# Performance work log

Hardware: AMD Instinct MI355X
Metric: run time of the kernel (lower is better)

## Reference

```python
import jax, jax.numpy as jnp
import numpy as np

N_NODES = 50000
N_EDGES = 800000
FEAT = 128
HID = 128
NUM_GRAPHS = 64
ODE_STEPS = 8   # fixed-step RK4 stand-in for adaptive odeint over CFG.ode_time_points
DEPTH = 1.0
EPS = 1e-5


def layer_norm(x, g, b):
    m = jnp.mean(x, axis=-1, keepdims=True)
    v = jnp.var(x, axis=-1, keepdims=True)
    return (x - m) * jax.lax.rsqrt(v + EPS) * g + b


def setup_inputs() -> dict:
    key = jax.random.key(0)
    ks = jax.random.split(key, 16)
    s = 1.0 / np.sqrt(FEAT)
    sh = 1.0 / np.sqrt(HID)
    inp = {
        "x": jax.random.normal(ks[0], (N_NODES, FEAT), jnp.float32),
        "edge_index": jax.random.randint(ks[1], (2, N_EDGES), 0, N_NODES, jnp.int64),
        "batch": jnp.sort(jax.random.randint(ks[2], (N_NODES,), 0, NUM_GRAPHS, jnp.int64)),
        "alpha": jnp.float32(0.8),
        "beta": jnp.float32(0.6),
        "phase": jnp.float32(0.7),
        "W_in": jax.random.normal(ks[3], (FEAT, HID), jnp.float32) * s,
        "b_in": jnp.zeros((HID,), jnp.float32),
        "g_in": jnp.ones((HID,), jnp.float32),
        "be_in": jnp.zeros((HID,), jnp.float32),
        "W_alt": jax.random.normal(ks[4], (FEAT, HID), jnp.float32) * s,
        "b_alt": jnp.zeros((HID,), jnp.float32),
        "g_alt": jnp.ones((HID,), jnp.float32),
        "be_alt": jnp.zeros((HID,), jnp.float32),
        "W_self": jax.random.normal(ks[5], (HID, HID), jnp.float32) * sh,
        "W_msg": jax.random.normal(ks[6], (HID, HID), jnp.float32) * sh,
        "b_ode": jnp.zeros((HID,), jnp.float32),
        "W_int": jax.random.normal(ks[7], (2 * HID, HID), jnp.float32) * sh / np.sqrt(2.0),
        "b_int": jnp.zeros((HID,), jnp.float32),
        "g_int": jnp.ones((HID,), jnp.float32),
        "be_int": jnp.zeros((HID,), jnp.float32),
        "W_out": jax.random.normal(ks[8], (HID, HID), jnp.float32) * sh,
        "b_out": jnp.zeros((HID,), jnp.float32),
    }
    return inp


def _forward(x, alpha, beta, phase,
             W_in, b_in, g_in, be_in,
             W_alt, b_alt, g_alt, be_alt,
             W_self, W_msg, b_ode,
             W_int, b_int, g_int, be_int,
             W_out, b_out,
             edge_index, batch):
    src, dst = edge_index[0], edge_index[1]
    # in-degree for mean aggregation (clamped to 1)
    deg = jax.ops.segment_sum(jnp.ones((src.shape[0],), jnp.float32), dst,
                              num_segments=N_NODES)
    deg = jnp.maximum(deg, 1.0)[:, None]

    # quantum amplitudes -> measurement probabilities (normalized)
    norm = jnp.sqrt(alpha ** 2 + beta ** 2)
    a, b = alpha / norm, beta / norm
    p0, p1 = a ** 2, b ** 2

    # two projection pathways in superposition
    h0 = jax.nn.gelu(layer_norm(x @ W_in + b_in, g_in, be_in))
    h1 = jax.nn.gelu(layer_norm(x @ W_alt + b_alt, g_alt, be_alt))
    h = jnp.sqrt(p0) * h0 + jnp.sqrt(p1) * h1  # [N, H]

    # Neural ODE: dh/dt = tanh(h W_self + mean_{j->i}(h_j W_msg) + b)
    def ode_f(h):
        msg = h[src] @ W_msg                       # [E, H] gather + GEMM
        agg = jax.ops.segment_sum(msg, dst, num_segments=N_NODES) / deg
        return jnp.tanh(h @ W_self + agg + b_ode)

    dt = jnp.float32(DEPTH / ODE_STEPS)

    def rk4_step(h, _):
        k1 = ode_f(h)
        k2 = ode_f(h + 0.5 * dt * k1)
        k3 = ode_f(h + 0.5 * dt * k2)
        k4 = ode_f(h + dt * k3)
        return h + (dt / 6.0) * (k1 + 2.0 * k2 + 2.0 * k3 + k4), None

    h, _ = jax.lax.scan(rk4_step, h, None, length=ODE_STEPS)

    # quantum interference mixing (conditional branch -> masked add)
    interf = 2.0 * jnp.sqrt(p0 * p1) * jnp.cos(phase)
    h_int = jnp.tanh(layer_norm(jnp.concatenate([h, h], axis=-1) @ W_int + b_int,
                                g_int, be_int))
    gate = jnp.where(jnp.abs(interf) > 0.01, interf, 0.0)
    h = h + gate * h_int

    # eval-mode collapse: if p1 >= p0, scale by Re(e^{i*phase}) = cos(phase)
    h = jnp.where(p0 > p1, h, h * jnp.cos(phase))

    h_out = h @ W_out + b_out

    # global mean pool over graphs
    cnt = jax.ops.segment_sum(jnp.ones((N_NODES,), jnp.float32), batch,
                              num_segments=NUM_GRAPHS)
    pooled = jax.ops.segment_sum(h_out, batch, num_segments=NUM_GRAPHS)
    return pooled / jnp.maximum(cnt, 1.0)[:, None]  # [NUM_GRAPHS, H]


def reference(x, edge_index, batch, alpha, beta, phase,
              W_in, b_in, g_in, be_in,
              W_alt, b_alt, g_alt, be_alt,
              W_self, W_msg, b_ode,
              W_int, b_int, g_int, be_int,
              W_out, b_out):
    return _forward(x, alpha, beta, phase,
                    W_in, b_in, g_in, be_in,
                    W_alt, b_alt, g_alt, be_alt,
                    W_self, W_msg, b_ode,
                    W_int, b_int, g_int, be_int,
                    W_out, b_out, edge_index, batch)
```

## Files before the change

kernel.cpp:

```cpp
#include <hip/hip_runtime.h>
#include <math.h>

#define NND 50000
#define NED 800000
#define HD  128
#define NG  64
#define MT  32

typedef __attribute__((ext_vector_type(8))) short short8v;
typedef __attribute__((ext_vector_type(4))) float float4v;
typedef __attribute__((ext_vector_type(2))) float float2v;

__device__ __forceinline__ float gelu_t(float x) {
  const float c = 0.7978845608028654f;
  float t = tanhf(c * (x + 0.044715f * x * x * x));
  return 0.5f * x * (1.0f + t);
}

__device__ __forceinline__ unsigned short f2bf(float f) {
  unsigned int u = __float_as_uint(f);
  u += 0x7FFFu + ((u >> 16) & 1u);
  return (unsigned short)(u >> 16);
}
__device__ __forceinline__ float bf2f(unsigned short s) {
  return __uint_as_float(((unsigned int)s) << 16);
}
__device__ __forceinline__ float bflo(unsigned int u) { return __uint_as_float(u << 16); }
__device__ __forceinline__ float bfhi(unsigned int u) { return __uint_as_float(u & 0xFFFF0000u); }
__device__ __forceinline__ unsigned char f2fp8(float f) {
  return (unsigned char)(__builtin_amdgcn_cvt_pk_fp8_f32(f, f, 0, false) & 0xFF);
}

__global__ void k_hist(const int* __restrict__ dst, int* __restrict__ degi) {
  int e = blockIdx.x * 256 + threadIdx.x;
  if (e < NED) atomicAdd(&degi[dst[e]], 1);
}

__global__ __launch_bounds__(1024) void k_scan(
    const int* __restrict__ degi, int* __restrict__ rowptr,
    int* __restrict__ cursor, float* __restrict__ deginv) {
  __shared__ int wsum[16];
  int tid = threadIdx.x;
  int lane = tid & 63;
  int wid = tid >> 6;
  int running = 0;
  for (int base = 0; base < NND; base += 1024) {
    int idx = base + tid;
    int v = (idx < NND) ? degi[idx] : 0;
    int s = v;
#pragma unroll
    for (int o = 1; o < 64; o <<= 1) {
      int t = __shfl_up(s, o, 64);
      if (lane >= o) s += t;
    }
    if (lane == 63) wsum[wid] = s;
    __syncthreads();
    if (wid == 0) {
      int ws = (lane < 16) ? wsum[lane] : 0;
#pragma unroll
      for (int o = 1; o < 16; o <<= 1) {
        int t = __shfl_up(ws, o, 64);
        if (lane >= o) ws += t;
      }
      if (lane < 16) wsum[lane] = ws;
    }
    __syncthreads();
    int woff = wid ? wsum[wid - 1] : 0;
    int excl = running + woff + s - v;
    if (idx < NND) {
      rowptr[idx] = excl;
      cursor[idx] = excl;
      deginv[idx] = 1.0f / (float)max(v, 1);
    }
    int tot = wsum[15];
    __syncthreads();
    running += tot;
  }
  if (tid == 0) rowptr[NND] = running;
}

__global__ void k_scatter(const int* __restrict__ src, const int* __restrict__ dst,
                          int* __restrict__ cursor, unsigned short* __restrict__ cs16) {
  int e = blockIdx.x * 256 + threadIdx.x;
  if (e < NED) {
    int d = dst[e];
    int pos = atomicAdd(&cursor[d], 1);
    cs16[pos] = (unsigned short)src[e];
  }
}

__global__ void k_cnt(const int* __restrict__ batch, float* __restrict__ cnt) {
  int g = threadIdx.x;
  if (g >= NG) return;
  int lo, hi, ub_g, ub_gm1;
  lo = 0; hi = NND;
  while (lo < hi) { int mid = (lo + hi) >> 1; if (batch[mid] <= g) lo = mid + 1; else hi = mid; }
  ub_g = lo;
  if (g == 0) ub_gm1 = 0;
  else {
    lo = 0; hi = NND;
    int v = g - 1;
    while (lo < hi) { int mid = (lo + hi) >> 1; if (batch[mid] <= v) lo = mid + 1; else hi = mid; }
    ub_gm1 = lo;
  }
  cnt[g] = (float)(ub_g - ub_gm1);
}

__global__ void k_weff(const float* __restrict__ Wint, float* __restrict__ weff) {
  int i = blockIdx.x * 256 + threadIdx.x;
  if (i < HD * HD) weff[i] = Wint[i] + Wint[i + HD * HD];
}

__global__ void k_prepB(const float* __restrict__ Wself, const float* __restrict__ Wmsg,
                        unsigned short* __restrict__ Bt) {
  int i = blockIdx.x * 256 + threadIdx.x;
  if (i < 128 * 256) {
    int n = i >> 8, k = i & 255;
    float w = (k < HD) ? Wself[k * HD + n] : Wmsg[(k - HD) * HD + n];
    Bt[i] = f2bf(w);
  }
}

__global__ void k_prepIn(const float* __restrict__ Win, const float* __restrict__ Walt,
                         unsigned short* __restrict__ BtIn) {
  int i = blockIdx.x * 256 + threadIdx.x;
  if (i < 2 * 128 * 128) {
    int p = i >> 14; int rem = i & 16383; int n = rem >> 7; int k = rem & 127;
    const float* W = p ? Walt : Win;
    BtIn[i] = f2bf(W[k * 128 + n]);
  }
}

__global__ __launch_bounds__(256) void k_init2(
    const float* __restrict__ x, const unsigned short* __restrict__ BtIn,
    const float* __restrict__ bin, const float* __restrict__ gin, const float* __restrict__ bein,
    const float* __restrict__ balt, const float* __restrict__ galt, const float* __restrict__ bealt,
    const float* __restrict__ alphap, const float* __restrict__ betap,
    unsigned short* __restrict__ hbf)
{
  __shared__ float red[4][16][2];
  __shared__ unsigned short gtile[2][16][64];
  int tid = threadIdx.x;
  int wave = tid >> 6;
  int lane = tid & 63;
  int l15 = lane & 15;
  int lhi = lane >> 4;
  int path = wave >> 1;
  int colBase = (wave & 1) * 64;
  int rowBase = blockIdx.x * 64;

  const unsigned short* Bp = BtIn + path * 128 * 128;
  short8v bfr[4][4];
#pragma unroll
  for (int t = 0; t < 4; ++t) {
    int n = colBase + t * 16 + l15;
#pragma unroll
    for (int s = 0; s < 4; ++s)
      bfr[t][s] = *(const short8v*)&Bp[n * 128 + s * 32 + lhi * 8];
  }

  const float* bvp = path ? balt : bin;
  const float* gp  = path ? galt : gin;
  const float* bep = path ? bealt : bein;
  float bv[4], gw[4], bew[4];
#pragma unroll
  for (int t = 0; t < 4; ++t) {
    int col = colBase + t * 16 + l15;
    bv[t] = bvp[col]; gw[t] = gp[col]; bew[t] = bep[col];
  }

  float al = alphap[0], btv = betap[0];
  float nrm = sqrtf(al * al + btv * btv);
  float w0 = fabsf(al) / nrm, w1 = fabsf(btv) / nrm;

  for (int rt = 0; rt < 4; ++rt) {
    int arow = rowBase + rt * 16 + l15; if (arow >= NND) arow = NND - 1;
    short8v afr[4];
#pragma unroll
    for (int s = 0; s < 4; ++s) {
      float4 xa = *(const float4*)&x[(size_t)arow * HD + s * 32 + lhi * 8];
      float4 xb = *(const float4*)&x[(size_t)arow * HD + s * 32 + lhi * 8 + 4];
      short8v f;
      f[0] = (short)f2bf(xa.x); f[1] = (short)f2bf(xa.y);
      f[2] = (short)f2bf(xa.z); f[3] = (short)f2bf(xa.w);
      f[4] = (short)f2bf(xb.x); f[5] = (short)f2bf(xb.y);
      f[6] = (short)f2bf(xb.z); f[7] = (short)f2bf(xb.w);
      afr[s] = f;
    }

    float4v acc[4];
#pragma unroll
    for (int t = 0; t < 4; ++t) acc[t] = (float4v){0.f, 0.f, 0.f, 0.f};
#pragma unroll
    for (int s = 0; s < 4; ++s) {
#pragma unroll
      for (int t = 0; t < 4; ++t)
        acc[t] = __builtin_amdgcn_mfma_f32_16x16x32_bf16(afr[s], bfr[t][s], acc[t], 0, 0, 0);
    }

    float z[4][4];
    float psum[4], psq[4];
#pragma unroll
    for (int r = 0; r < 4; ++r) {
      float s1 = 0.f, s2 = 0.f;
#pragma unroll
      for (int t = 0; t < 4; ++t) {
        float zz = acc[t][r] + bv[t];
        z[r][t] = zz;
        s1 += zz; s2 += zz * zz;
      }
#pragma unroll
      for (int m = 1; m < 16; m <<= 1) {
        s1 += __shfl_xor(s1, m, 16);
        s2 += __shfl_xor(s2, m, 16);
      }
      psum[r] = s1; psq[r] = s2;
    }
    if (l15 == 0) {
#pragma unroll
      for (int r = 0; r < 4; ++r) {
        red[wave][lhi * 4 + r][0] = psum[r];
        red[wave][lhi * 4 + r][1] = psq[r];
      }
    }
    __syncthreads();

    int pw = wave ^ 1;
    float gval[4][4];
#pragma unroll
    for (int r = 0; r < 4; ++r) {
      int rowl = lhi * 4 + r;
      float S = psum[r] + red[pw][rowl][0];
      float Q = psq[r]  + red[pw][rowl][1];
      float mean = S * (1.0f / 128.0f);
      float var  = Q * (1.0f / 128.0f) - mean * mean;
      float rs = rsqrtf(var + 1e-5f);
#pragma unroll
      for (int t = 0; t < 4; ++t)
        gval[r][t] = gelu_t((z[r][t] - mean) * rs * gw[t] + bew[t]);
    }

    if (path == 1) {
#pragma unroll
      for (int r = 0; r < 4; ++r)
#pragma unroll
        for (int t = 0; t < 4; ++t)
          gtile[wave & 1][lhi * 4 + r][t * 16 + l15] = f2bf(gval[r][t]);
    }
    __syncthreads();

    if (path == 0) {
#pragma unroll
      for (int r = 0; r < 4; ++r) {
        int m = rowBase + rt * 16 + lhi * 4 + r;
        if (m < NND) {
#pragma unroll
          for (int t = 0; t < 4; ++t) {
            float g1 = bf2f(gtile[wave & 1][lhi * 4 + r][t * 16 + l15]);
            float hv = w0 * gval[r][t] + w1 * g1;
            hbf[(size_t)m * HD + colBase + t * 16 + l15] = f2bf(hv);
          }
        }
      }
    }
    __syncthreads();
  }
}

__global__ __launch_bounds__(256) void k_gath2(
    const unsigned short* __restrict__ hbf,
    const unsigned char*  __restrict__ t8,
    unsigned short* __restrict__ usav,
    unsigned short* __restrict__ uT,
    const int* __restrict__ rowptr,
    const unsigned short* __restrict__ cs16,
    const float* __restrict__ deginv,
    int mode, float cu)
{
  int tid = threadIdx.x;
  int l16 = tid & 15;
  int grp = tid >> 4;
  int node = blockIdx.x * 16 + grp;
  if (node >= NND) return;
  int e0 = rowptr[node], e1 = rowptr[node + 1];
  float a0=0,a1=0,a2=0,a3=0,a4=0,a5=0,a6=0,a7=0;

  if (mode == 0) {
    for (int eb = e0; eb < e1; eb += 16) {
      int rem = e1 - eb;
      int ia = eb + l16; if (ia > e1 - 1) ia = e1 - 1;
      int my = cs16[ia];
      int n16 = (rem < 16) ? rem : 16;
#pragma unroll
      for (int j = 0; j < 16; ++j) {
        if (j < n16) {
          int s = __shfl(my, j, 16);
          uint4 v = *(const uint4*)&hbf[(size_t)s * HD + l16 * 8];
          a0 += bflo(v.x); a1 += bfhi(v.x); a2 += bflo(v.y); a3 += bfhi(v.y);
          a4 += bflo(v.z); a5 += bfhi(v.z); a6 += bflo(v.w); a7 += bfhi(v.w);
        }
      }
    }
  } else {
    for (int eb = e0; eb < e1; eb += 16) {
      int rem = e1 - eb;
      int ia = eb + l16; if (ia > e1 - 1) ia = e1 - 1;
      int my = cs16[ia];
      int n16 = (rem < 16) ? rem : 16;
      uint2 v[16];
#pragma unroll
      for (int j = 0; j < 16; ++j) {
        if (j < n16) {
          int s = __shfl(my, j, 16);
          v[j] = *(const uint2*)&t8[(size_t)s * HD + l16 * 8];
        }
      }
#pragma unroll
      for (int j = 0; j < 16; ++j) {
        if (j < n16) {
          float2v f0 = __builtin_amdgcn_cvt_pk_f32_fp8(v[j].x, false);
          float2v f1 = __builtin_amdgcn_cvt_pk_f32_fp8(v[j].x, true);
          float2v f2 = __builtin_amdgcn_cvt_pk_f32_fp8(v[j].y, false);
          float2v f3 = __builtin_amdgcn_cvt_pk_f32_fp8(v[j].y, true);
          a0 += f0[0]; a1 += f0[1]; a2 += f1[0]; a3 += f1[1];
          a4 += f2[0]; a5 += f2[1]; a6 += f3[0]; a7 += f3[1];
        }
      }
    }
  }

  float sc = deginv[node] * ((mode == 0) ? 1.0f : ((mode == 1) ? 0.125f : cu));
  size_t base = (size_t)node * HD + l16 * 8;
  float u0,u1,u2,u3,u4,u5,u6,u7;
  if (mode == 0) {
    u0=a0*sc; u1=a1*sc; u2=a2*sc; u3=a3*sc; u4=a4*sc; u5=a5*sc; u6=a6*sc; u7=a7*sc;
  } else {
    uint4 us = *(const uint4*)&usav[base];
    u0 = bflo(us.x) + a0*sc; u1 = bfhi(us.x) + a1*sc;
    u2 = bflo(us.y) + a2*sc; u3 = bfhi(us.y) + a3*sc;
    u4 = bflo(us.z) + a4*sc; u5 = bfhi(us.z) + a5*sc;
    u6 = bflo(us.w) + a6*sc; u7 = bfhi(us.w) + a7*sc;
  }
  uint4 o;
  o.x = (unsigned int)f2bf(u0) | ((unsigned int)f2bf(u1) << 16);
  o.y = (unsigned int)f2bf(u2) | ((unsigned int)f2bf(u3) << 16);
  o.z = (unsigned int)f2bf(u4) | ((unsigned int)f2bf(u5) << 16);
  o.w = (unsigned int)f2bf(u6) | ((unsigned int)f2bf(u7) << 16);
  if (mode <= 1) *(uint4*)&usav[base] = o;
  *(uint4*)&uT[base] = o;
}

__global__ __launch_bounds__(256) void k_ode2(
    const unsigned short* __restrict__ ain,
    unsigned short* __restrict__ hbf,
    const unsigned short* __restrict__ uT,
    unsigned char* __restrict__ k8w,
    unsigned char* __restrict__ dh8,
    unsigned short* __restrict__ kacc,
    const unsigned short* __restrict__ Bt, const float* __restrict__ bode,
    unsigned short* __restrict__ ybf, int stage)
{
  int tid = threadIdx.x;
  int wave = tid >> 6;
  int lane = tid & 63;
  int l15 = lane & 15;
  int lhi = lane >> 4;
  int rowBase = blockIdx.x * MT;
  int ncol0 = wave * 32;

  const float DT = 0.125f;
  const float wk = (stage == 0 || stage == 3) ? DT / 6.0f : DT / 3.0f;
  const float cy = (stage <= 1) ? 0.5f * DT : DT;

  short8v bfr[2][8];
#pragma unroll
  for (int t = 0; t < 2; ++t) {
    int n = ncol0 + t * 16 + l15;
#pragma unroll
    for (int s = 0; s < 8; ++s) {
      bfr[t][s] = *(const short8v*)&Bt[n * 256 + s * 32 + lhi * 8];
    }
  }
  float4 bo4[2];
  bo4[0] = *(const float4*)&bode[ncol0 + lhi * 4];
  bo4[1] = *(const float4*)&bode[ncol0 + 16 + lhi * 4];

#pragma unroll
  for (int rt = 0; rt < MT / 16; ++rt) {
    int mload = rowBase + rt * 16 + l15;
    if (mload >= NND) mload = NND - 1;
    short8v afr[8];
#pragma unroll
    for (int s = 0; s < 4; ++s)
      afr[s] = *(const short8v*)&ain[(size_t)mload * HD + s * 32 + lhi * 8];
#pragma unroll
    for (int s = 0; s < 4; ++s)
      afr[4 + s] = *(const short8v*)&uT[(size_t)mload * HD + s * 32 + lhi * 8];

    float4v acc0 = {0.f, 0.f, 0.f, 0.f};
    float4v acc1 = {0.f, 0.f, 0.f, 0.f};
#pragma unroll
    for (int s = 0; s < 8; ++s) {
      acc0 = __builtin_amdgcn_mfma_f32_16x16x32_bf16(bfr[0][s], afr[s], acc0, 0, 0, 0);
      acc1 = __builtin_amdgcn_mfma_f32_16x16x32_bf16(bfr[1][s], afr[s], acc1, 0, 0, 0);
    }

    int m = rowBase + rt * 16 + l15;
    if (m < NND) {
#pragma unroll
      for (int t = 0; t < 2; ++t) {
        int n0 = ncol0 + t * 16 + lhi * 4;
        size_t off = (size_t)m * HD + n0;
        float4v acc = t ? acc1 : acc0;
        float4 bo = bo4[t];
        float kv0 = tanhf(acc[0] + bo.x);
        float kv1 = tanhf(acc[1] + bo.y);
        float kv2 = tanhf(acc[2] + bo.z);
        float kv3 = tanhf(acc[3] + bo.w);
        if (stage < 3) {
          uint2 hv = *(const uint2*)&hbf[off];
          float y0 = bflo(hv.x) + cy * kv0;
          float y1 = bfhi(hv.x) + cy * kv1;
          float y2 = bflo(hv.y) + cy * kv2;
          float y3 = bfhi(hv.y) + cy * kv3;
          uint2 yo;
          yo.x = (unsigned int)f2bf(y0) | ((unsigned int)f2bf(y1) << 16);
          yo.y = (unsigned int)f2bf(y2) | ((unsigned int)f2bf(y3) << 16);
          *(uint2*)&ybf[off] = yo;
          float k0 = wk * kv0, k1 = wk * kv1, k2 = wk * kv2, k3 = wk * kv3;
          if (stage > 0) {
            uint2 ka = *(const uint2*)&kacc[off];
            k0 += bflo(ka.x); k1 += bfhi(ka.x);
            k2 += bflo(ka.y); k3 += bfhi(ka.y);
          }
          uint2 ko;
          ko.x = (unsigned int)f2bf(k0) | ((unsigned int)f2bf(k1) << 16);
          ko.y = (unsigned int)f2bf(k2) | ((unsigned int)f2bf(k3) << 16);
          *(uint2*)&kacc[off] = ko;
          unsigned int p8 = __builtin_amdgcn_cvt_pk_fp8_f32(kv0, kv1, 0u, false);
          p8 = __builtin_amdgcn_cvt_pk_fp8_f32(kv2, kv3, p8, true);
          *(unsigned int*)&k8w[off] = p8;
        } else {
          uint2 ka = *(const uint2*)&kacc[off];
          float dh0 = bflo(ka.x) + wk * kv0;
          float dh1 = bfhi(ka.x) + wk * kv1;
          float dh2 = bflo(ka.y) + wk * kv2;
          float dh3 = bfhi(ka.y) + wk * kv3;
          uint2 hv = *(const uint2*)&hbf[off];
          float h0 = bflo(hv.x) + dh0;
          float h1 = bfhi(hv.x) + dh1;
          float h2 = bflo(hv.y) + dh2;
          float h3 = bfhi(hv.y) + dh3;
          uint2 ho;
          ho.x = (unsigned int)f2bf(h0) | ((unsigned int)f2bf(h1) << 16);
          ho.y = (unsigned int)f2bf(h2) | ((unsigned int)f2bf(h3) << 16);
          *(uint2*)&hbf[off] = ho;
          unsigned int p8 = __builtin_amdgcn_cvt_pk_fp8_f32(8.0f * dh0, 8.0f * dh1, 0u, false);
          p8 = __builtin_amdgcn_cvt_pk_fp8_f32(8.0f * dh2, 8.0f * dh3, p8, true);
          *(unsigned int*)&dh8[off] = p8;
        }
      }
    }
  }
}

__global__ __launch_bounds__(256) void k_interf(
    const unsigned short* __restrict__ hbf, const float* __restrict__ weff,
    const float* __restrict__ bint, const float* __restrict__ gint,
    const float* __restrict__ beint,
    const float* __restrict__ alphap, const float* __restrict__ betap,
    const float* __restrict__ phasep,
    float* __restrict__ h2out)
{
  __shared__ float As[64][16];
  __shared__ float Bs[16][128];
  int tid = threadIdx.x;
  int tx = tid & 31, ty = tid >> 5;
  int rowBase = blockIdx.x * 64;
  float acc[8][4];
#pragma unroll
  for (int i = 0; i < 8; ++i) { acc[i][0]=0.f; acc[i][1]=0.f; acc[i][2]=0.f; acc[i][3]=0.f; }

  for (int kc = 0; kc < 8; ++kc) {
    int k0 = kc * 16;
    {
      int r = tid >> 2, kq = (tid & 3) * 4;
      int row = rowBase + r; if (row >= NND) row = NND - 1;
      uint2 v = *(const uint2*)&hbf[(size_t)row * HD + k0 + kq];
      As[r][kq+0] = bflo(v.x); As[r][kq+1] = bfhi(v.x);
      As[r][kq+2] = bflo(v.y); As[r][kq+3] = bfhi(v.y);
    }
#pragma unroll
    for (int j = 0; j < 2; ++j) {
      int kk = (tid >> 5) + j * 8;
      int n = (tid & 31) * 4;
      *(float4*)&Bs[kk][n] = *(const float4*)&weff[(k0 + kk) * HD + n];
    }
    __syncthreads();
#pragma unroll
    for (int kq = 0; kq < 4; ++kq) {
      float4 b0 = *(float4*)&Bs[kq*4+0][tx*4];
      float4 b1 = *(float4*)&Bs[kq*4+1][tx*4];
      float4 b2 = *(float4*)&Bs[kq*4+2][tx*4];
      float4 b3 = *(float4*)&Bs[kq*4+3][tx*4];
#pragma unroll
      for (int i = 0; i < 8; ++i) {
        float4 a = *(float4*)&As[ty*8+i][kq*4];
        acc[i][0] = fmaf(a.x,b0.x,fmaf(a.y,b1.x,fmaf(a.z,b2.x,fmaf(a.w,b3.x,acc[i][0]))));
        acc[i][1] = fmaf(a.x,b0.y,fmaf(a.y,b1.y,fmaf(a.z,b2.y,fmaf(a.w,b3.y,acc[i][1]))));
        acc[i][2] = fmaf(a.x,b0.z,fmaf(a.y,b1.z,fmaf(a.z,b2.z,fmaf(a.w,b3.z,acc[i][2]))));
        acc[i][3] = fmaf(a.x,b0.w,fmaf(a.y,b1.w,fmaf(a.z,b2.w,fmaf(a.w,b3.w,acc[i][3]))));
      }
    }
    __syncthreads();
  }

  float al = alphap[0], bt = betap[0], ph = phasep[0];
  float n2 = al*al + bt*bt;
  float p0 = (al*al) / n2, p1 = (bt*bt) / n2;
  float interf = 2.0f * sqrtf(p0 * p1) * cosf(ph);
  float gate = (fabsf(interf) > 0.01f) ? interf : 0.0f;
  float cscale = (p0 > p1) ? 1.0f : cosf(ph);

  int c0 = tx * 4;
  float4 bi  = *(const float4*)&bint[c0];
  float4 gv  = *(const float4*)&gint[c0];
  float4 bev = *(const float4*)&beint[c0];
#pragma unroll
  for (int i = 0; i < 8; ++i) {
    int row = rowBase + ty*8 + i;
    float z0 = acc[i][0]+bi.x, z1 = acc[i][1]+bi.y, z2 = acc[i][2]+bi.z, z3 = acc[i][3]+bi.w;
    float rsum = z0+z1+z2+z3;
    float rsq  = z0*z0+z1*z1+z2*z2+z3*z3;
#pragma unroll
    for (int m = 1; m < 32; m <<= 1) { rsum += __shfl_xor(rsum, m, 32); rsq += __shfl_xor(rsq, m, 32); }
    float mean = rsum * (1.0f/128.0f);
    float var  = rsq * (1.0f/128.0f) - mean*mean;
    float rs = rsqrtf(var + 1e-5f);
    float t0 = tanhf((z0-mean)*rs*gv.x + bev.x);
    float t1 = tanhf((z1-mean)*rs*gv.y + bev.y);
    float t2 = tanhf((z2-mean)*rs*gv.z + bev.z);
    float t3 = tanhf((z3-mean)*rs*gv.w + bev.w);
    if (row < NND) {
      size_t off = (size_t)row * HD + c0;
      uint2 hv = *(const uint2*)&hbf[off];
      float h0 = bflo(hv.x), h1 = bfhi(hv.x), h2 = bflo(hv.y), h3 = bfhi(hv.y);
      float4 o = make_float4((h0 + gate*t0) * cscale,
                             (h1 + gate*t1) * cscale,
                             (h2 + gate*t2) * cscale,
                             (h3 + gate*t3) * cscale);
      *(float4*)&h2out[off] = o;
    }
  }
}

__global__ __launch_bounds__(256) void k_out(
    const float* __restrict__ h2, const float* __restrict__ Wout,
    const float* __restrict__ bout, const int* __restrict__ batch,
    float* __restrict__ pooled)
{
  __shared__ float As[64][16];
  __shared__ float Bs[16][128];
  int tid = threadIdx.x;
  int tx = tid & 31, ty = tid >> 5;
  int rowBase = blockIdx.x * 64;
  float acc[8][4];
#pragma unroll
  for (int i = 0; i < 8; ++i) { acc[i][0]=0.f; acc[i][1]=0.f; acc[i][2]=0.f; acc[i][3]=0.f; }

  for (int kc = 0; kc < 8; ++kc) {
    int k0 = kc * 16;
    {
      int r = tid >> 2, kq = (tid & 3) * 4;
      int row = rowBase + r; if (row >= NND) row = NND - 1;
      *(float4*)&As[r][kq] = *(const float4*)&h2[(size_t)row * HD + k0 + kq];
    }
#pragma unroll
    for (int j = 0; j < 2; ++j) {
      int kk = (tid >> 5) + j * 8;
      int n = (tid & 31) * 4;
      *(float4*)&Bs[kk][n] = *(const float4*)&Wout[(k0 + kk) * HD + n];
    }
    __syncthreads();
#pragma unroll
    for (int kq = 0; kq < 4; ++kq) {
      float4 b0 = *(float4*)&Bs[kq*4+0][tx*4];
      float4 b1 = *(float4*)&Bs[kq*4+1][tx*4];
      float4 b2 = *(float4*)&Bs[kq*4+2][tx*4];
      float4 b3 = *(float4*)&Bs[kq*4+3][tx*4];
#pragma unroll
      for (int i = 0; i < 8; ++i) {
        float4 a = *(float4*)&As[ty*8+i][kq*4];
        acc[i][0] = fmaf(a.x,b0.x,fmaf(a.y,b1.x,fmaf(a.z,b2.x,fmaf(a.w,b3.x,acc[i][0]))));
        acc[i][1] = fmaf(a.x,b0.y,fmaf(a.y,b1.y,fmaf(a.z,b2.y,fmaf(a.w,b3.y,acc[i][1]))));
        acc[i][2] = fmaf(a.x,b0.z,fmaf(a.y,b1.z,fmaf(a.z,b2.z,fmaf(a.w,b3.z,acc[i][2]))));
        acc[i][3] = fmaf(a.x,b0.w,fmaf(a.y,b1.w,fmaf(a.z,b2.w,fmaf(a.w,b3.w,acc[i][3]))));
      }
    }
    __syncthreads();
  }

  int c0 = tx * 4;
  float4 bo = *(const float4*)&bout[c0];
  int prevg = -1;
  float r0 = 0.f, r1 = 0.f, r2 = 0.f, r3 = 0.f;
#pragma unroll
  for (int i = 0; i < 8; ++i) {
    int row = rowBase + ty*8 + i;
    if (row >= NND) break;
    int g = batch[row];
    float v0 = acc[i][0] + bo.x;
    float v1 = acc[i][1] + bo.y;
    float v2 = acc[i][2] + bo.z;
    float v3 = acc[i][3] + bo.w;
    if (g != prevg) {
      if (prevg >= 0) {
        atomicAdd(&pooled[prevg*HD + c0 + 0], r0);
        atomicAdd(&pooled[prevg*HD + c0 + 1], r1);
        atomicAdd(&pooled[prevg*HD + c0 + 2], r2);
        atomicAdd(&pooled[prevg*HD + c0 + 3], r3);
      }
      prevg = g; r0 = v0; r1 = v1; r2 = v2; r3 = v3;
    } else {
      r0 += v0; r1 += v1; r2 += v2; r3 += v3;
    }
  }
  if (prevg >= 0) {
    atomicAdd(&pooled[prevg*HD + c0 + 0], r0);
    atomicAdd(&pooled[prevg*HD + c0 + 1], r1);
    atomicAdd(&pooled[prevg*HD + c0 + 2], r2);
    atomicAdd(&pooled[prevg*HD + c0 + 3], r3);
  }
}

__global__ void k_final(const float* __restrict__ pooled, const float* __restrict__ cnt,
                        float* __restrict__ out) {
  int i = blockIdx.x * 256 + threadIdx.x;
  if (i < NG * HD) out[i] = pooled[i] / fmaxf(cnt[i >> 7], 1.0f);
}

extern "C" void kernel_launch(void* const* d_in, const int* in_sizes, int n_in,
                              void* d_out, int out_size, void* d_ws, size_t ws_size,
                              hipStream_t stream) {
  (void)in_sizes; (void)n_in; (void)out_size; (void)ws_size;
  const float* x     = (const float*)d_in[0];
  const int*   ei    = (const int*)d_in[1];
  const int*   batch = (const int*)d_in[2];
  const float* alpha = (const float*)d_in[3];
  const float* beta  = (const float*)d_in[4];
  const float* phase = (const float*)d_in[5];
  const float* Win   = (const float*)d_in[6];
  const float* bin   = (const float*)d_in[7];
  const float* gin   = (const float*)d_in[8];
  const float* bein  = (const float*)d_in[9];
  const float* Walt  = (const float*)d_in[10];
  const float* balt  = (const float*)d_in[11];
  const float* galt  = (const float*)d_in[12];
  const float* bealt = (const float*)d_in[13];
  const float* Wself = (const float*)d_in[14];
  const float* Wmsg  = (const float*)d_in[15];
  const float* bode  = (const float*)d_in[16];
  const float* Wint  = (const float*)d_in[17];
  const float* bint  = (const float*)d_in[18];
  const float* gint  = (const float*)d_in[19];
  const float* beint = (const float*)d_in[20];
  const float* Wout  = (const float*)d_in[21];
  const float* bout  = (const float*)d_in[22];
  float* out = (float*)d_out;

  const int* esrc = ei;
  const int* edst = ei + NED;

  size_t NH = (size_t)NND * HD;
  float* h2     = (float*)d_ws;
  float* deginv = h2 + NH;
  float* weff   = deginv + NND;
  float* pooled = weff + HD * HD;
  float* cnt    = pooled + NG * HD;
  unsigned short* hbf  = (unsigned short*)(cnt + NG);
  unsigned short* ybf  = hbf + NH;
  unsigned short* kacc = ybf + NH;
  unsigned short* usav = kacc + NH;
  unsigned short* uT   = usav + NH;
  unsigned short* Bt   = uT + NH;
  unsigned short* BtIn = Bt + 128 * 256;
  unsigned short* cs16 = BtIn + 2 * 128 * 128;
  unsigned char* k8a = (unsigned char*)(cs16 + NED);
  unsigned char* k8b = k8a + NH;
  unsigned char* dh8 = k8b + NH;
  int* degi   = (int*)(dh8 + NH);
  int* rowptr = degi + NND;
  int* cursor = rowptr + (NND + 4);

  hipMemsetAsync(degi, 0, NND * sizeof(int), stream);
  hipMemsetAsync(pooled, 0, NG * HD * sizeof(float), stream);

  k_hist   <<<(NED + 255) / 256, 256, 0, stream>>>(edst, degi);
  k_scan   <<<1, 1024, 0, stream>>>(degi, rowptr, cursor, deginv);
  k_scatter<<<(NED + 255) / 256, 256, 0, stream>>>(esrc, edst, cursor, cs16);
  k_cnt    <<<1, 64, 0, stream>>>(batch, cnt);
  k_weff   <<<(HD * HD + 255) / 256, 256, 0, stream>>>(Wint, weff);
  k_prepB  <<<128, 256, 0, stream>>>(Wself, Wmsg, Bt);
  k_prepIn <<<128, 256, 0, stream>>>(Win, Walt, BtIn);
  k_init2  <<<(NND + 63) / 64, 256, 0, stream>>>(x, BtIn, bin, gin, bein,
                                                 balt, galt, bealt,
                                                 alpha, beta, hbf);

  const float DT = 0.125f;
  int gg = (NND + 15) / 16;
  int ob = (NND + MT - 1) / MT;
  for (int step = 0; step < 8; ++step) {
    k_gath2<<<gg, 256, 0, stream>>>(hbf, dh8, usav, uT, rowptr, cs16, deginv,
                                    (step == 0) ? 0 : 1, 0.f);
    k_ode2 <<<ob, 256, 0, stream>>>(hbf, hbf, uT, k8a, dh8, kacc, Bt, bode, ybf, 0);
    k_gath2<<<gg, 256, 0, stream>>>(hbf, k8a, usav, uT, rowptr, cs16, deginv, 2, 0.5f * DT);
    k_ode2 <<<ob, 256, 0, stream>>>(ybf, hbf, uT, k8b, dh8, kacc, Bt, bode, ybf, 1);
    k_gath2<<<gg, 256, 0, stream>>>(hbf, k8b, usav, uT, rowptr, cs16, deginv, 2, 0.5f * DT);
    k_ode2 <<<ob, 256, 0, stream>>>(ybf, hbf, uT, k8a, dh8, kacc, Bt, bode, ybf, 2);
    k_gath2<<<gg, 256, 0, stream>>>(hbf, k8a, usav, uT, rowptr, cs16, deginv, 2, DT);
    k_ode2 <<<ob, 256, 0, stream>>>(ybf, hbf, uT, k8b, dh8, kacc, Bt, bode, ybf, 3);
  }
  k_interf<<<(NND + 63) / 64, 256, 0, stream>>>(hbf, weff, bint, gint, beint,
                                                alpha, beta, phase, h2);
  k_out   <<<(NND + 63) / 64, 256, 0, stream>>>(h2, Wout, bout, batch, pooled);
  k_final <<<(NG * HD + 255) / 256, 256, 0, stream>>>(pooled, cnt, out);
}
```

Before: 2.203 ms.

## Use MFMA for interference/output GEMMs and drop bf16 RK4 accumulator

The interference and output projections move from fp32 LDS-tiled FMA loops to bf16 MFMA kernels, with transposed bf16 weights prepared up front. The intermediate h2 is stored in bf16, and pooling first reduces into per-block LDS slots before issuing global atomics. Separately, the RK4 stages stop reading and writing a bf16 k accumulator. Instead the final stage recombines the three stored fp8 stage slopes, which cuts per-stage memory traffic at the cost of lower-precision slope accumulation.

```diff
diff --git a/kernel.cpp b/kernel.cpp
--- a/kernel.cpp
+++ b/kernel.cpp
@@ -27,9 +27,6 @@
 }
 __device__ __forceinline__ float bflo(unsigned int u) { return __uint_as_float(u << 16); }
 __device__ __forceinline__ float bfhi(unsigned int u) { return __uint_as_float(u & 0xFFFF0000u); }
-__device__ __forceinline__ unsigned char f2fp8(float f) {
-  return (unsigned char)(__builtin_amdgcn_cvt_pk_fp8_f32(f, f, 0, false) & 0xFF);
-}
 
 __global__ void k_hist(const int* __restrict__ dst, int* __restrict__ degi) {
   int e = blockIdx.x * 256 + threadIdx.x;
@@ -106,9 +103,20 @@
   cnt[g] = (float)(ub_g - ub_gm1);
 }
 
-__global__ void k_weff(const float* __restrict__ Wint, float* __restrict__ weff) {
+__global__ void k_weffT(const float* __restrict__ Wint, unsigned short* __restrict__ weffT) {
   int i = blockIdx.x * 256 + threadIdx.x;
-  if (i < HD * HD) weff[i] = Wint[i] + Wint[i + HD * HD];
+  if (i < 128 * 128) {
+    int n = i >> 7, k = i & 127;
+    weffT[i] = f2bf(Wint[k * 128 + n] + Wint[(k + 128) * 128 + n]);
+  }
+}
+
+__global__ void k_prepOut(const float* __restrict__ Wout, unsigned short* __restrict__ WoutT) {
+  int i = blockIdx.x * 256 + threadIdx.x;
+  if (i < 128 * 128) {
+    int n = i >> 7, k = i & 127;
+    WoutT[i] = f2bf(Wout[k * 128 + n]);
+  }
 }
 
 __global__ void k_prepB(const float* __restrict__ Wself, const float* __restrict__ Wmsg,
@@ -355,8 +363,10 @@
     unsigned short* __restrict__ hbf,
     const unsigned short* __restrict__ uT,
     unsigned char* __restrict__ k8w,
+    const unsigned char* __restrict__ k8r0,
+    const unsigned char* __restrict__ k8r1,
+    const unsigned char* __restrict__ k8r2,
     unsigned char* __restrict__ dh8,
-    unsigned short* __restrict__ kacc,
     const unsigned short* __restrict__ Bt, const float* __restrict__ bode,
     unsigned short* __restrict__ ybf, int stage)
 {
@@ -369,8 +379,8 @@
   int ncol0 = wave * 32;
 
   const float DT = 0.125f;
-  const float wk = (stage == 0 || stage == 3) ? DT / 6.0f : DT / 3.0f;
   const float cy = (stage <= 1) ? 0.5f * DT : DT;
+  const float w6 = DT / 6.0f;
 
   short8v bfr[2][8];
 #pragma unroll
@@ -427,25 +437,23 @@
           yo.x = (unsigned int)f2bf(y0) | ((unsigned int)f2bf(y1) << 16);
           yo.y = (unsigned int)f2bf(y2) | ((unsigned int)f2bf(y3) << 16);
           *(uint2*)&ybf[off] = yo;
-          float k0 = wk * kv0, k1 = wk * kv1, k2 = wk * kv2, k3 = wk * kv3;
-          if (stage > 0) {
-            uint2 ka = *(const uint2*)&kacc[off];
-            k0 += bflo(ka.x); k1 += bfhi(ka.x);
-            k2 += bflo(ka.y); k3 += bfhi(ka.y);
-          }
-          uint2 ko;
-          ko.x = (unsigned int)f2bf(k0) | ((unsigned int)f2bf(k1) << 16);
-          ko.y = (unsigned int)f2bf(k2) | ((unsigned int)f2bf(k3) << 16);
-          *(uint2*)&kacc[off] = ko;
           unsigned int p8 = __builtin_amdgcn_cvt_pk_fp8_f32(kv0, kv1, 0u, false);
           p8 = __builtin_amdgcn_cvt_pk_fp8_f32(kv2, kv3, p8, true);
           *(unsigned int*)&k8w[off] = p8;
         } else {
-          uint2 ka = *(const uint2*)&kacc[off];
-          float dh0 = bflo(ka.x) + wk * kv0;
-          float dh1 = bfhi(ka.x) + wk * kv1;
-          float dh2 = bflo(ka.y) + wk * kv2;
-          float dh3 = bfhi(ka.y) + wk * kv3;
+          unsigned int q0 = *(const unsigned int*)&k8r0[off];
+          unsigned int q1 = *(const unsigned int*)&k8r1[off];
+          unsigned int q2 = *(const unsigned int*)&k8r2[off];
+          float2v a0 = __builtin_amdgcn_cvt_pk_f32_fp8(q0, false);
+          float2v a1 = __builtin_amdgcn_cvt_pk_f32_fp8(q0, true);
+          float2v b0 = __builtin_amdgcn_cvt_pk_f32_fp8(q1, false);
+          float2v b1 = __builtin_amdgcn_cvt_pk_f32_fp8(q1, true);
+          float2v c0 = __builtin_amdgcn_cvt_pk_f32_fp8(q2, false);
+          float2v c1 = __builtin_amdgcn_cvt_pk_f32_fp8(q2, true);
+          float dh0 = w6 * (a0[0] + 2.f * b0[0] + 2.f * c0[0] + kv0);
+          float dh1 = w6 * (a0[1] + 2.f * b0[1] + 2.f * c0[1] + kv1);
+          float dh2 = w6 * (a1[0] + 2.f * b1[0] + 2.f * c1[0] + kv2);
+          float dh3 = w6 * (a1[1] + 2.f * b1[1] + 2.f * c1[1] + kv3);
           uint2 hv = *(const uint2*)&hbf[off];
           float h0 = bflo(hv.x) + dh0;
           float h1 = bfhi(hv.x) + dh1;
@@ -464,55 +472,38 @@
   }
 }
 
-__global__ __launch_bounds__(256) void k_interf(
-    const unsigned short* __restrict__ hbf, const float* __restrict__ weff,
+__global__ __launch_bounds__(256) void k_interf2(
+    const unsigned short* __restrict__ hbf, const unsigned short* __restrict__ weffT,
     const float* __restrict__ bint, const float* __restrict__ gint,
     const float* __restrict__ beint,
     const float* __restrict__ alphap, const float* __restrict__ betap,
     const float* __restrict__ phasep,
-    float* __restrict__ h2out)
+    unsigned short* __restrict__ h2bf)
 {
-  __shared__ float As[64][16];
-  __shared__ float Bs[16][128];
+  __shared__ float red[4][16][2];
   int tid = threadIdx.x;
-  int tx = tid & 31, ty = tid >> 5;
-  int rowBase = blockIdx.x * 64;
-  float acc[8][4];
-#pragma unroll
-  for (int i = 0; i < 8; ++i) { acc[i][0]=0.f; acc[i][1]=0.f; acc[i][2]=0.f; acc[i][3]=0.f; }
-
-  for (int kc = 0; kc < 8; ++kc) {
-    int k0 = kc * 16;
-    {
-      int r = tid >> 2, kq = (tid & 3) * 4;
-      int row = rowBase + r; if (row >= NND) row = NND - 1;
-      uint2 v = *(const uint2*)&hbf[(size_t)row * HD + k0 + kq];
-      As[r][kq+0] = bflo(v.x); As[r][kq+1] = bfhi(v.x);
-      As[r][kq+2] = bflo(v.y); As[r][kq+3] = bfhi(v.y);
-    }
-#pragma unroll
-    for (int j = 0; j < 2; ++j) {
-      int kk = (tid >> 5) + j * 8;
-      int n = (tid & 31) * 4;
-      *(float4*)&Bs[kk][n] = *(const float4*)&weff[(k0 + kk) * HD + n];
-    }
-    __syncthreads();
-#pragma unroll
-    for (int kq = 0; kq < 4; ++kq) {
-      float4 b0 = *(float4*)&Bs[kq*4+0][tx*4];
-      float4 b1 = *(float4*)&Bs[kq*4+1][tx*4];
-      float4 b2 = *(float4*)&Bs[kq*4+2][tx*4];
-      float4 b3 = *(float4*)&Bs[kq*4+3][tx*4];
-#pragma unroll
-      for (int i = 0; i < 8; ++i) {
-        float4 a = *(float4*)&As[ty*8+i][kq*4];
-        acc[i][0] = fmaf(a.x,b0.x,fmaf(a.y,b1.x,fmaf(a.z,b2.x,fmaf(a.w,b3.x,acc[i][0]))));
-        acc[i][1] = fmaf(a.x,b0.y,fmaf(a.y,b1.y,fmaf(a.z,b2.y,fmaf(a.w,b3.y,acc[i][1]))));
-        acc[i][2] = fmaf(a.x,b0.z,fmaf(a.y,b1.z,fmaf(a.z,b2.z,fmaf(a.w,b3.z,acc[i][2]))));
-        acc[i][3] = fmaf(a.x,b0.w,fmaf(a.y,b1.w,fmaf(a.z,b2.w,fmaf(a.w,b3.w,acc[i][3]))));
-      }
-    }
-    __syncthreads();
+  int wave = tid >> 6;
+  int lane = tid & 63;
+  int l15 = lane & 15;
+  int lhi = lane >> 4;
+  int rowBase = blockIdx.x * 32;
+  int ncol0 = wave * 32;
+
+  short8v bfr[2][4];
+#pragma unroll
+  for (int t = 0; t < 2; ++t) {
+    int n = ncol0 + t * 16 + l15;
+#pragma unroll
+    for (int s = 0; s < 4; ++s)
+      bfr[t][s] = *(const short8v*)&weffT[n * 128 + s * 32 + lhi * 8];
+  }
+  float4 bi4[2], gv4[2], bev4[2];
+#pragma unroll
+  for (int t = 0; t < 2; ++t) {
+    int n0 = ncol0 + t * 16 + lhi * 4;
+    bi4[t]  = *(const float4*)&bint[n0];
+    gv4[t]  = *(const float4*)&gint[n0];
+    bev4[t] = *(const float4*)&beint[n0];
   }
 
   float al = alphap[0], bt = betap[0], ph = phasep[0];
@@ -522,115 +513,141 @@
   float gate = (fabsf(interf) > 0.01f) ? interf : 0.0f;
   float cscale = (p0 > p1) ? 1.0f : cosf(ph);
 
-  int c0 = tx * 4;
-  float4 bi  = *(const float4*)&bint[c0];
-  float4 gv  = *(const float4*)&gint[c0];
-  float4 bev = *(const float4*)&beint[c0];
-#pragma unroll
-  for (int i = 0; i < 8; ++i) {
-    int row = rowBase + ty*8 + i;
-    float z0 = acc[i][0]+bi.x, z1 = acc[i][1]+bi.y, z2 = acc[i][2]+bi.z, z3 = acc[i][3]+bi.w;
-    float rsum = z0+z1+z2+z3;
-    float rsq  = z0*z0+z1*z1+z2*z2+z3*z3;
-#pragma unroll
-    for (int m = 1; m < 32; m <<= 1) { rsum += __shfl_xor(rsum, m, 32); rsq += __shfl_xor(rsq, m, 32); }
-    float mean = rsum * (1.0f/128.0f);
-    float var  = rsq * (1.0f/128.0f) - mean*mean;
+  for (int rt = 0; rt < 2; ++rt) {
+    int mload = rowBase + rt * 16 + l15;
+    if (mload >= NND) mload = NND - 1;
+    short8v afr[4];
+#pragma unroll
+    for (int s = 0; s < 4; ++s)
+      afr[s] = *(const short8v*)&hbf[(size_t)mload * HD + s * 32 + lhi * 8];
+
+    float4v acc0 = {0.f, 0.f, 0.f, 0.f};
+    float4v acc1 = {0.f, 0.f, 0.f, 0.f};
+#pragma unroll
+    for (int s = 0; s < 4; ++s) {
+      acc0 = __builtin_amdgcn_mfma_f32_16x16x32_bf16(bfr[0][s], afr[s], acc0, 0, 0, 0);
+      acc1 = __builtin_amdgcn_mfma_f32_16x16x32_bf16(bfr[1][s], afr[s], acc1, 0, 0, 0);
+    }
+
+    float z[2][4];
+    float s1 = 0.f, s2 = 0.f;
+#pragma unroll
+    for (int t = 0; t < 2; ++t) {
+      float4v acc = t ? acc1 : acc0;
+#pragma unroll
+      for (int i = 0; i < 4; ++i) {
+        float zz = acc[i] + ((const float*)&bi4[t])[i];
+        z[t][i] = zz;
+        s1 += zz; s2 += zz * zz;
+      }
+    }
+    s1 += __shfl_xor(s1, 16, 64); s2 += __shfl_xor(s2, 16, 64);
+    s1 += __shfl_xor(s1, 32, 64); s2 += __shfl_xor(s2, 32, 64);
+    if (lhi == 0) { red[wave][l15][0] = s1; red[wave][l15][1] = s2; }
+    __syncthreads();
+    float S = red[0][l15][0] + red[1][l15][0] + red[2][l15][0] + red[3][l15][0];
+    float Q = red[0][l15][1] + red[1][l15][1] + red[2][l15][1] + red[3][l15][1];
+    float mean = S * (1.0f / 128.0f);
+    float var  = Q * (1.0f / 128.0f) - mean * mean;
     float rs = rsqrtf(var + 1e-5f);
-    float t0 = tanhf((z0-mean)*rs*gv.x + bev.x);
-    float t1 = tanhf((z1-mean)*rs*gv.y + bev.y);
-    float t2 = tanhf((z2-mean)*rs*gv.z + bev.z);
-    float t3 = tanhf((z3-mean)*rs*gv.w + bev.w);
-    if (row < NND) {
-      size_t off = (size_t)row * HD + c0;
-      uint2 hv = *(const uint2*)&hbf[off];
-      float h0 = bflo(hv.x), h1 = bfhi(hv.x), h2 = bflo(hv.y), h3 = bfhi(hv.y);
-      float4 o = make_float4((h0 + gate*t0) * cscale,
-                             (h1 + gate*t1) * cscale,
-                             (h2 + gate*t2) * cscale,
-                             (h3 + gate*t3) * cscale);
-      *(float4*)&h2out[off] = o;
-    }
-  }
-}
-
-__global__ __launch_bounds__(256) void k_out(
-    const float* __restrict__ h2, const float* __restrict__ Wout,
+
+    int m = rowBase + rt * 16 + l15;
+    if (m < NND) {
+#pragma unroll
+      for (int t = 0; t < 2; ++t) {
+        size_t off = (size_t)m * HD + ncol0 + t * 16 + lhi * 4;
+        uint2 hv = *(const uint2*)&hbf[off];
+        float h0 = bflo(hv.x), h1 = bfhi(hv.x), h2 = bflo(hv.y), h3 = bfhi(hv.y);
+        float t0 = tanhf((z[t][0]-mean)*rs*((const float*)&gv4[t])[0] + ((const float*)&bev4[t])[0]);
+        float t1 = tanhf((z[t][1]-mean)*rs*((const float*)&gv4[t])[1] + ((const float*)&bev4[t])[1]);
+        float t2 = tanhf((z[t][2]-mean)*rs*((const float*)&gv4[t])[2] + ((const float*)&bev4[t])[2]);
+        float t3 = tanhf((z[t][3]-mean)*rs*((const float*)&gv4[t])[3] + ((const float*)&bev4[t])[3]);
+        float o0 = (h0 + gate*t0) * cscale;
+        float o1 = (h1 + gate*t1) * cscale;
+        float o2 = (h2 + gate*t2) * cscale;
+        float o3 = (h3 + gate*t3) * cscale;
+        uint2 oo;
+        oo.x = (unsigned int)f2bf(o0) | ((unsigned int)f2bf(o1) << 16);
+        oo.y = (unsigned int)f2bf(o2) | ((unsigned int)f2bf(o3) << 16);
+        *(uint2*)&h2bf[off] = oo;
+      }
+    }
+    __syncthreads();
+  }
+}
+
+__global__ __launch_bounds__(256) void k_out2(
+    const unsigned short* __restrict__ h2bf, const unsigned short* __restrict__ WoutT,
     const float* __restrict__ bout, const int* __restrict__ batch,
     float* __restrict__ pooled)
 {
-  __shared__ float As[64][16];
-  __shared__ float Bs[16][128];
+  __shared__ float lpool[2][128];
+  __shared__ int lgid[2];
   int tid = threadIdx.x;
-  int tx = tid & 31, ty = tid >> 5;
-  int rowBase = blockIdx.x * 64;
-  float acc[8][4];
-#pragma unroll
-  for (int i = 0; i < 8; ++i) { acc[i][0]=0.f; acc[i][1]=0.f; acc[i][2]=0.f; acc[i][3]=0.f; }
-
-  for (int kc = 0; kc < 8; ++kc) {
-    int k0 = kc * 16;
-    {
-      int r = tid >> 2, kq = (tid & 3) * 4;
-      int row = rowBase + r; if (row >= NND) row = NND - 1;
-      *(float4*)&As[r][kq] = *(const float4*)&h2[(size_t)row * HD + k0 + kq];
-    }
-#pragma unroll
-    for (int j = 0; j < 2; ++j) {
-      int kk = (tid >> 5) + j * 8;
-      int n = (tid & 31) * 4;
-      *(float4*)&Bs[kk][n] = *(const float4*)&Wout[(k0 + kk) * HD + n];
-    }
-    __syncthreads();
-#pragma unroll
-    for (int kq = 0; kq < 4; ++kq) {
-      float4 b0 = *(float4*)&Bs[kq*4+0][tx*4];
-      float4 b1 = *(float4*)&Bs[kq*4+1][tx*4];
-      float4 b2 = *(float4*)&Bs[kq*4+2][tx*4];
-      float4 b3 = *(float4*)&Bs[kq*4+3][tx*4];
-#pragma unroll
-      for (int i = 0; i < 8; ++i) {
-        float4 a = *(float4*)&As[ty*8+i][kq*4];
-        acc[i][0] = fmaf(a.x,b0.x,fmaf(a.y,b1.x,fmaf(a.z,b2.x,fmaf(a.w,b3.x,acc[i][0]))));
-        acc[i][1] = fmaf(a.x,b0.y,fmaf(a.y,b1.y,fmaf(a.z,b2.y,fmaf(a.w,b3.y,acc[i][1]))));
-        acc[i][2] = fmaf(a.x,b0.z,fmaf(a.y,b1.z,fmaf(a.z,b2.z,fmaf(a.w,b3.z,acc[i][2]))));
-        acc[i][3] = fmaf(a.x,b0.w,fmaf(a.y,b1.w,fmaf(a.z,b2.w,fmaf(a.w,b3.w,acc[i][3]))));
-      }
-    }
-    __syncthreads();
-  }
-
-  int c0 = tx * 4;
-  float4 bo = *(const float4*)&bout[c0];
-  int prevg = -1;
-  float r0 = 0.f, r1 = 0.f, r2 = 0.f, r3 = 0.f;
-#pragma unroll
-  for (int i = 0; i < 8; ++i) {
-    int row = rowBase + ty*8 + i;
-    if (row >= NND) break;
-    int g = batch[row];
-    float v0 = acc[i][0] + bo.x;
-    float v1 = acc[i][1] + bo.y;
-    float v2 = acc[i][2] + bo.z;
-    float v3 = acc[i][3] + bo.w;
-    if (g != prevg) {
-      if (prevg >= 0) {
-        atomicAdd(&pooled[prevg*HD + c0 + 0], r0);
-        atomicAdd(&pooled[prevg*HD + c0 + 1], r1);
-        atomicAdd(&pooled[prevg*HD + c0 + 2], r2);
-        atomicAdd(&pooled[prevg*HD + c0 + 3], r3);
-      }
-      prevg = g; r0 = v0; r1 = v1; r2 = v2; r3 = v3;
-    } else {
-      r0 += v0; r1 += v1; r2 += v2; r3 += v3;
-    }
-  }
-  if (prevg >= 0) {
-    atomicAdd(&pooled[prevg*HD + c0 + 0], r0);
-    atomicAdd(&pooled[prevg*HD + c0 + 1], r1);
-    atomicAdd(&pooled[prevg*HD + c0 + 2], r2);
-    atomicAdd(&pooled[prevg*HD + c0 + 3], r3);
-  }
+  int wave = tid >> 6;
+  int lane = tid & 63;
+  int l15 = lane & 15;
+  int lhi = lane >> 4;
+  int rowBase = blockIdx.x * 32;
+  int ncol0 = wave * 32;
+
+  lpool[tid >> 7][tid & 127] = 0.f;
+  if (tid == 0) {
+    lgid[0] = batch[rowBase < NND ? rowBase : NND - 1];
+    int last = rowBase + 31; if (last >= NND) last = NND - 1;
+    lgid[1] = batch[last];
+  }
+  __syncthreads();
+
+  short8v bfr[2][4];
+#pragma unroll
+  for (int t = 0; t < 2; ++t) {
+    int n = ncol0 + t * 16 + l15;
+#pragma unroll
+    for (int s = 0; s < 4; ++s)
+      bfr[t][s] = *(const short8v*)&WoutT[n * 128 + s * 32 + lhi * 8];
+  }
+  float4 bo4[2];
+  bo4[0] = *(const float4*)&bout[ncol0 + lhi * 4];
+  bo4[1] = *(const float4*)&bout[ncol0 + 16 + lhi * 4];
+
+#pragma unroll
+  for (int rt = 0; rt < 2; ++rt) {
+    int mload = rowBase + rt * 16 + l15;
+    if (mload >= NND) mload = NND - 1;
+    short8v afr[4];
+#pragma unroll
+    for (int s = 0; s < 4; ++s)
+      afr[s] = *(const short8v*)&h2bf[(size_t)mload * HD + s * 32 + lhi * 8];
+
+    float4v acc0 = {0.f, 0.f, 0.f, 0.f};
+    float4v acc1 = {0.f, 0.f, 0.f, 0.f};
+#pragma unroll
+    for (int s = 0; s < 4; ++s) {
+      acc0 = __builtin_amdgcn_mfma_f32_16x16x32_bf16(bfr[0][s], afr[s], acc0, 0, 0, 0);
+      acc1 = __builtin_amdgcn_mfma_f32_16x16x32_bf16(bfr[1][s], afr[s], acc1, 0, 0, 0);
+    }
+
+    int m = rowBase + rt * 16 + l15;
+    if (m < NND) {
+      int g = batch[m];
+      int slot = (g == lgid[0]) ? 0 : 1;
+#pragma unroll
+      for (int t = 0; t < 2; ++t) {
+        int n0 = ncol0 + t * 16 + lhi * 4;
+        float4v acc = t ? acc1 : acc0;
+        float4 bo = bo4[t];
+        atomicAdd(&lpool[slot][n0 + 0], acc[0] + bo.x);
+        atomicAdd(&lpool[slot][n0 + 1], acc[1] + bo.y);
+        atomicAdd(&lpool[slot][n0 + 2], acc[2] + bo.z);
+        atomicAdd(&lpool[slot][n0 + 3], acc[3] + bo.w);
+      }
+    }
+  }
+  __syncthreads();
+  int slot = tid >> 7, col = tid & 127;
+  if (slot == 0 || lgid[1] != lgid[0])
+    atomicAdd(&pooled[lgid[slot] * HD + col], lpool[slot][col]);
 }
 
 __global__ void k_final(const float* __restrict__ pooled, const float* __restrict__ cnt,
@@ -672,22 +689,23 @@
   const int* edst = ei + NED;
 
   size_t NH = (size_t)NND * HD;
-  float* h2     = (float*)d_ws;
-  float* deginv = h2 + NH;
-  float* weff   = deginv + NND;
-  float* pooled = weff + HD * HD;
+  float* deginv = (float*)d_ws;
+  float* pooled = deginv + NND;
   float* cnt    = pooled + NG * HD;
-  unsigned short* hbf  = (unsigned short*)(cnt + NG);
-  unsigned short* ybf  = hbf + NH;
-  unsigned short* kacc = ybf + NH;
-  unsigned short* usav = kacc + NH;
-  unsigned short* uT   = usav + NH;
-  unsigned short* Bt   = uT + NH;
-  unsigned short* BtIn = Bt + 128 * 256;
-  unsigned short* cs16 = BtIn + 2 * 128 * 128;
-  unsigned char* k8a = (unsigned char*)(cs16 + NED);
-  unsigned char* k8b = k8a + NH;
-  unsigned char* dh8 = k8b + NH;
+  unsigned short* hbf   = (unsigned short*)(cnt + NG);
+  unsigned short* ybf   = hbf + NH;
+  unsigned short* usav  = ybf + NH;
+  unsigned short* uT    = usav + NH;
+  unsigned short* h2bf  = uT + NH;
+  unsigned short* Bt    = h2bf + NH;
+  unsigned short* BtIn  = Bt + 128 * 256;
+  unsigned short* weffT = BtIn + 2 * 128 * 128;
+  unsigned short* WoutT = weffT + 128 * 128;
+  unsigned short* cs16  = WoutT + 128 * 128;
+  unsigned char* k80 = (unsigned char*)(cs16 + NED);
+  unsigned char* k81 = k80 + NH;
+  unsigned char* k82 = k81 + NH;
+  unsigned char* dh8 = k82 + NH;
   int* degi   = (int*)(dh8 + NH);
   int* rowptr = degi + NND;
   int* cursor = rowptr + (NND + 4);
@@ -699,7 +717,8 @@
   k_scan   <<<1, 1024, 0, stream>>>(degi, rowptr, cursor, deginv);
   k_scatter<<<(NED + 255) / 256, 256, 0, stream>>>(esrc, edst, cursor, cs16);
   k_cnt    <<<1, 64, 0, stream>>>(batch, cnt);
-  k_weff   <<<(HD * HD + 255) / 256, 256, 0, stream>>>(Wint, weff);
+  k_weffT  <<<64, 256, 0, stream>>>(Wint, weffT);
+  k_prepOut<<<64, 256, 0, stream>>>(Wout, WoutT);
   k_prepB  <<<128, 256, 0, stream>>>(Wself, Wmsg, Bt);
   k_prepIn <<<128, 256, 0, stream>>>(Win, Walt, BtIn);
   k_init2  <<<(NND + 63) / 64, 256, 0, stream>>>(x, BtIn, bin, gin, bein,
@@ -712,16 +731,20 @@
   for (int step = 0; step < 8; ++step) {
     k_gath2<<<gg, 256, 0, stream>>>(hbf, dh8, usav, uT, rowptr, cs16, deginv,
                                     (step == 0) ? 0 : 1, 0.f);
-    k_ode2 <<<ob, 256, 0, stream>>>(hbf, hbf, uT, k8a, dh8, kacc, Bt, bode, ybf, 0);
-    k_gath2<<<gg, 256, 0, stream>>>(hbf, k8a, usav, uT, rowptr, cs16, deginv, 2, 0.5f * DT);
-    k_ode2 <<<ob, 256, 0, stream>>>(ybf, hbf, uT, k8b, dh8, kacc, Bt, bode, ybf, 1);
-    k_gath2<<<gg, 256, 0, stream>>>(hbf, k8b, usav, uT, rowptr, cs16, deginv, 2, 0.5f * DT);
-    k_ode2 <<<ob, 256, 0, stream>>>(ybf, hbf, uT, k8a, dh8, kacc, Bt, bode, ybf, 2);
-    k_gath2<<<gg, 256, 0, stream>>>(hbf, k8a, usav, uT, rowptr, cs16, deginv, 2, DT);
-    k_ode2 <<<ob, 256, 0, stream>>>(ybf, hbf, uT, k8b, dh8, kacc, Bt, bode, ybf, 3);
-  }
-  k_interf<<<(NND + 63) / 64, 256, 0, stream>>>(hbf, weff, bint, gint, beint,
-                                                alpha, beta, phase, h2);
-  k_out   <<<(NND + 63) / 64, 256, 0, stream>>>(h2, Wout, bout, batch, pooled);
+    k_ode2 <<<ob, 256, 0, stream>>>(hbf, hbf, uT, k80, k80, k81, k82, dh8,
+                                    Bt, bode, ybf, 0);
+    k_gath2<<<gg, 256, 0, stream>>>(hbf, k80, usav, uT, rowptr, cs16, deginv, 2, 0.5f * DT);
+    k_ode2 <<<ob, 256, 0, stream>>>(ybf, hbf, uT, k81, k80, k81, k82, dh8,
+                                    Bt, bode, ybf, 1);
+    k_gath2<<<gg, 256, 0, stream>>>(hbf, k81, usav, uT, rowptr, cs16, deginv, 2, 0.5f * DT);
+    k_ode2 <<<ob, 256, 0, stream>>>(ybf, hbf, uT, k82, k80, k81, k82, dh8,
+                                    Bt, bode, ybf, 2);
+    k_gath2<<<gg, 256, 0, stream>>>(hbf, k82, usav, uT, rowptr, cs16, deginv, 2, DT);
+    k_ode2 <<<ob, 256, 0, stream>>>(ybf, hbf, uT, k80, k80, k81, k82, dh8,
+                                    Bt, bode, ybf, 3);
+  }
+  k_interf2<<<(NND + 31) / 32, 256, 0, stream>>>(hbf, weffT, bint, gint, beint,
+                                                 alpha, beta, phase, h2bf);
+  k_out2  <<<(NND + 31) / 32, 256, 0, stream>>>(h2bf, WoutT, bout, batch, pooled);
   k_final <<<(NG * HD + 255) / 256, 256, 0, stream>>>(pooled, cnt, out);
 }
```

Result: faster. 2.150 ms (-2.4%).
